# Kernel optimization log

Measured on AMD Instinct MI355X. Metric: run time of the kernel, lower is better.

The kernel has to match this reference:

```python
import jax, jax.numpy as jnp
import numpy as np

OUT = 7            # output_size
SR = 2             # sampling_ratio
SCALES = (0.25, 0.125, 0.0625, 0.03125)   # FPN strides 4,8,16,32
K_MIN, K_MAX = 2, 5
CANON_SCALE = 224.0
CANON_LVL = 4.0
EPS = 1e-6


def setup_inputs() -> dict:
    key = jax.random.key(0)
    ks = jax.random.split(key, 7)
    feat0 = jax.random.normal(ks[0], (2, 256, 200, 200), dtype=jnp.float32)
    feat1 = jax.random.normal(ks[1], (2, 256, 100, 100), dtype=jnp.float32)
    feat2 = jax.random.normal(ks[2], (2, 256, 50, 50), dtype=jnp.float32)
    feat3 = jax.random.normal(ks[3], (2, 256, 25, 25), dtype=jnp.float32)
    # boxes in 800x800 image coords: x1,y1 in [0,600), w,h in [2,200)
    xy = jax.random.uniform(ks[4], (2, 512, 2), dtype=jnp.float32) * 600.0
    wh = jax.random.uniform(ks[5], (2, 512, 2), dtype=jnp.float32) * 198.0 + 2.0
    boxes = jnp.concatenate([xy, xy + wh], axis=-1)  # [B,K,4] x1,y1,x2,y2
    return {"feat0": feat0, "feat1": feat1, "feat2": feat2, "feat3": feat3, "boxes": boxes}


def _bilinear(feat, bidx, ys, xs):
    # feat [B,C,H,W], bidx [N] int, ys [N,OY], xs [N,OX] -> [N,C,OY,OX]
    H, W = feat.shape[2], feat.shape[3]
    vy = (ys >= -1.0) & (ys <= float(H))
    vx = (xs >= -1.0) & (xs <= float(W))
    y = jnp.clip(ys, 0.0, H - 1.0)
    x = jnp.clip(xs, 0.0, W - 1.0)
    y0 = jnp.floor(y).astype(jnp.int32)
    x0 = jnp.floor(x).astype(jnp.int32)
    y1 = jnp.minimum(y0 + 1, H - 1)
    x1 = jnp.minimum(x0 + 1, W - 1)
    ly = y - y0
    lx = x - x0

    def g(yi, xi):
        # advanced indexing -> [N,OY,OX,C]
        return feat[bidx[:, None, None], :, yi[:, :, None], xi[:, None, :]]

    wy0 = (1.0 - ly)[:, :, None, None]
    wy1 = ly[:, :, None, None]
    wx0 = (1.0 - lx)[:, None, :, None]
    wx1 = lx[:, None, :, None]
    v = (wy0 * (wx0 * g(y0, x0) + wx1 * g(y0, x1))
         + wy1 * (wx0 * g(y1, x0) + wx1 * g(y1, x1)))
    v = v * (vy[:, :, None] & vx[:, None, :])[..., None].astype(v.dtype)
    return jnp.transpose(v, (0, 3, 1, 2))  # [N,C,OY,OX]


def _roi_align(feat, bidx, boxes, scale):
    # torchvision roi_align, aligned=False
    x1 = boxes[:, 0] * scale
    y1 = boxes[:, 1] * scale
    x2 = boxes[:, 2] * scale
    y2 = boxes[:, 3] * scale
    rw = jnp.maximum(x2 - x1, 1.0)
    rh = jnp.maximum(y2 - y1, 1.0)
    bw = rw / OUT
    bh = rh / OUT
    # flattened sample offsets: (j + 0.5)/SR in bin units, j in [0, OUT*SR)
    off = (jnp.arange(OUT * SR, dtype=jnp.float32) + 0.5) / SR
    ys = y1[:, None] + off[None, :] * bh[:, None]   # [N, OUT*SR]
    xs = x1[:, None] + off[None, :] * bw[:, None]   # [N, OUT*SR]
    v = _bilinear(feat, bidx, ys, xs)               # [N,C,OUT*SR,OUT*SR]
    N, C = v.shape[0], v.shape[1]
    v = v.reshape(N, C, OUT, SR, OUT, SR)
    return v.mean(axis=(3, 5))                      # [N,C,OUT,OUT]


def reference(feat0, feat1, feat2, feat3, boxes):
    feats = [feat0, feat1, feat2, feat3]
    B, K = boxes.shape[0], boxes.shape[1]
    boxes_f = boxes.reshape(-1, 4)                   # [N,4]
    bidx = jnp.repeat(jnp.arange(B, dtype=jnp.int32), K)
    # FPN level assignment (torchvision LevelMapper)
    area = (boxes_f[:, 2] - boxes_f[:, 0]) * (boxes_f[:, 3] - boxes_f[:, 1])
    lvl = jnp.floor(CANON_LVL + jnp.log2(jnp.sqrt(area) / CANON_SCALE + EPS))
    lvl = jnp.clip(lvl, K_MIN, K_MAX)
    idx = (lvl - K_MIN).astype(jnp.int32)            # [N] in {0..3}
    # compute ROI align at every level, select per box (jit-friendly)
    out = _roi_align(feats[0], bidx, boxes_f, SCALES[0])
    for l in range(1, 4):
        vl = _roi_align(feats[l], bidx, boxes_f, SCALES[l])
        out = jnp.where((idx == l)[:, None, None, None], vl, out)
    return out  # [B*K, C, 7, 7]
```

## Files before the change

kernel.cpp:

```cpp
#include <hip/hip_runtime.h>
#include <math.h>


constexpr int CH = 256;
constexpr int POUT = 7;
constexpr int NSAMP = 14;
constexpr int NBIN = POUT * POUT;
constexpr int PER_ROI = CH * NBIN;
constexpr int NWAVE = 2;
constexpr int CPW = 8;
constexpr int CPB = NWAVE * CPW;
constexpr int NCG = CH / CPB;

struct F2 { float x, y; };
__device__ inline F2 ld2(const float* p) { F2 v; __builtin_memcpy(&v, p, 8); return v; }
struct F4 { float x, y, z, w; };
__device__ inline F4 ld4(const float* p) { F4 v; __builtin_memcpy(&v, p, 16); return v; }

__global__ __launch_bounds__(128)
void roi_align_bin_kernel(const float* __restrict__ f0,
                          const float* __restrict__ f1,
                          const float* __restrict__ f2,
                          const float* __restrict__ f3,
                          const float* __restrict__ boxes,
                          float* __restrict__ out,
                          int K)
{
    __shared__ int   s_rowoff[2 * NSAMP];
    __shared__ float s_wy0[NSAMP], s_wy1[NSAMP];
    __shared__ int   s_xlc[NSAMP];
    __shared__ float s_ex0[NSAMP], s_ex1[NSAMP];

    const int tid  = threadIdx.x;
    const int wave = tid >> 6;
    const int lane = tid & 63;
    const int roi  = blockIdx.x >> 4;
    const int cg   = blockIdx.x & (NCG - 1);
    const int b    = roi / K;

    const float bx1 = boxes[roi * 4 + 0], by1 = boxes[roi * 4 + 1];
    const float bx2 = boxes[roi * 4 + 2], by2 = boxes[roi * 4 + 3];

    const float area = (bx2 - bx1) * (by2 - by1);
    float lvlf = floorf(4.0f + log2f(sqrtf(area) / 224.0f + 1e-6f));
    lvlf = fminf(fmaxf(lvlf, 2.0f), 5.0f);
    const int lvl = (int)lvlf - 2;

    const float* feat; int H, W; float scale;
    if (lvl == 0)      { feat = f0; H = 200; W = 200; scale = 0.25f;    }
    else if (lvl == 1) { feat = f1; H = 100; W = 100; scale = 0.125f;   }
    else if (lvl == 2) { feat = f2; H = 50;  W = 50;  scale = 0.0625f;  }
    else               { feat = f3; H = 25;  W = 25;  scale = 0.03125f; }

    const float x1 = bx1 * scale, y1 = by1 * scale;
    const float rw = fmaxf(bx2 * scale - x1, 1.0f);
    const float rh = fmaxf(by2 * scale - y1, 1.0f);
    const float bw = rw * (1.0f / POUT);
    const float bh = rh * (1.0f / POUT);

    if (tid < 2 * NSAMP) {
        const bool isY = tid < NSAMP;
        const int i = isY ? tid : tid - NSAMP;
        const float dim   = isY ? (float)H : (float)W;
        const float start = isY ? y1 : x1;
        const float bsz   = isY ? bh : bw;
        const float p = start + ((float)i + 0.5f) * 0.5f * bsz;
        const float valid = (p >= -1.0f && p <= dim) ? 1.0f : 0.0f;
        const float pc = fminf(fmaxf(p, 0.0f), dim - 1.0f);
        const int q0 = (int)floorf(pc);
        const float l = pc - (float)q0;
        const float w0 = (1.0f - l) * valid;
        const float w1 = l * valid;
        if (isY) {
            const int q1 = min(q0 + 1, (int)dim - 1);
            s_rowoff[2 * i]     = q0 * W;
            s_rowoff[2 * i + 1] = q1 * W;
            s_wy0[i] = w0;
            s_wy1[i] = w1;
        } else {
            const bool edge = (q0 > W - 2);
            s_xlc[i] = edge ? (W - 2) : q0;
            s_ex0[i] = edge ? 0.0f : w0;
            s_ex1[i] = edge ? (w1 + w0) : w1;
        }
    }
    __syncthreads();

    bool narrow = true;
    #pragma unroll
    for (int j = 0; j < POUT; ++j)
        narrow = narrow && (s_xlc[2 * j + 1] - s_xlc[2 * j] <= 2);

    const int  lp = (lane < NBIN) ? lane : (NBIN - 1);
    const bool act = (lane < NBIN);
    const int  by = lp / POUT, bx = lp - POUT * by;

    const int ro0 = s_rowoff[4 * by + 0];
    const int ro1 = s_rowoff[4 * by + 1];
    const int ro2 = s_rowoff[4 * by + 2];
    const int ro3 = s_rowoff[4 * by + 3];
    const float wy0 = s_wy0[2 * by],     wy1 = s_wy1[2 * by];
    const float wy2 = s_wy0[2 * by + 1], wy3 = s_wy1[2 * by + 1];

    const int lc0 = s_xlc[2 * bx], lc1 = s_xlc[2 * bx + 1];
    const float e00 = s_ex0[2 * bx],     e01 = s_ex1[2 * bx];
    const float e10 = s_ex0[2 * bx + 1], e11 = s_ex1[2 * bx + 1];

    const int HW = H * W;
    const int cbase = cg * CPB + wave * CPW;
    const float* chan0 = feat + ((size_t)b * CH + cbase) * (size_t)HW;
    const size_t obase = (size_t)roi * PER_ROI + (size_t)cbase * NBIN + lp;

    if (narrow) {
        const int base = min(lc0, W - 4);
        const int i0 = lc0 - base;
        const int i1 = lc1 - base;
        const float w40 = (i0 == 0 ? e00 : 0.0f) + (i1 == 0 ? e10 : 0.0f);
        const float w41 = (i0 == 1 ? e00 : 0.0f) + (i0 == 0 ? e01 : 0.0f)
                        + (i1 == 1 ? e10 : 0.0f) + (i1 == 0 ? e11 : 0.0f);
        const float w42 = (i0 == 2 ? e00 : 0.0f) + (i0 == 1 ? e01 : 0.0f)
                        + (i1 == 2 ? e10 : 0.0f) + (i1 == 1 ? e11 : 0.0f);
        const float w43 = (i0 == 2 ? e01 : 0.0f) + (i1 == 2 ? e11 : 0.0f);

        F4 v0 = ld4(chan0 + ro0 + base);
        F4 v1 = ld4(chan0 + ro1 + base);
        F4 v2 = ld4(chan0 + ro2 + base);
        F4 v3 = ld4(chan0 + ro3 + base);

        #pragma unroll
        for (int c = 0; c < CPW; ++c) {
            F4 n0, n1, n2, n3;
            if (c + 1 < CPW) {
                const float* ch = chan0 + (size_t)(c + 1) * HW;
                n0 = ld4(ch + ro0 + base);
                n1 = ld4(ch + ro1 + base);
                n2 = ld4(ch + ro2 + base);
                n3 = ld4(ch + ro3 + base);
            }
            const float rv0 = v0.x * w40 + v0.y * w41 + v0.z * w42 + v0.w * w43;
            const float rv1 = v1.x * w40 + v1.y * w41 + v1.z * w42 + v1.w * w43;
            const float rv2 = v2.x * w40 + v2.y * w41 + v2.z * w42 + v2.w * w43;
            const float rv3 = v3.x * w40 + v3.y * w41 + v3.z * w42 + v3.w * w43;
            const float acc = wy0 * rv0 + wy1 * rv1 + wy2 * rv2 + wy3 * rv3;
            if (act) out[obase + (size_t)c * NBIN] = acc * 0.25f;
            v0 = n0; v1 = n1; v2 = n2; v3 = n3;
        }
    } else {
        F2 a0 = ld2(chan0 + ro0 + lc0), d0 = ld2(chan0 + ro0 + lc1);
        F2 a1 = ld2(chan0 + ro1 + lc0), d1 = ld2(chan0 + ro1 + lc1);
        F2 a2 = ld2(chan0 + ro2 + lc0), d2 = ld2(chan0 + ro2 + lc1);
        F2 a3 = ld2(chan0 + ro3 + lc0), d3 = ld2(chan0 + ro3 + lc1);

        #pragma unroll
        for (int c = 0; c < CPW; ++c) {
            F2 na0, na1, na2, na3, nd0, nd1, nd2, nd3;
            if (c + 1 < CPW) {
                const float* ch = chan0 + (size_t)(c + 1) * HW;
                na0 = ld2(ch + ro0 + lc0); nd0 = ld2(ch + ro0 + lc1);
                na1 = ld2(ch + ro1 + lc0); nd1 = ld2(ch + ro1 + lc1);
                na2 = ld2(ch + ro2 + lc0); nd2 = ld2(ch + ro2 + lc1);
                na3 = ld2(ch + ro3 + lc0); nd3 = ld2(ch + ro3 + lc1);
            }
            const float rv0 = e00 * a0.x + e01 * a0.y + e10 * d0.x + e11 * d0.y;
            const float rv1 = e00 * a1.x + e01 * a1.y + e10 * d1.x + e11 * d1.y;
            const float rv2 = e00 * a2.x + e01 * a2.y + e10 * d2.x + e11 * d2.y;
            const float rv3 = e00 * a3.x + e01 * a3.y + e10 * d3.x + e11 * d3.y;
            const float acc = wy0 * rv0 + wy1 * rv1 + wy2 * rv2 + wy3 * rv3;
            if (act) out[obase + (size_t)c * NBIN] = acc * 0.25f;
            a0 = na0; a1 = na1; a2 = na2; a3 = na3;
            d0 = nd0; d1 = nd1; d2 = nd2; d3 = nd3;
        }
    }
}

extern "C" void kernel_launch(void* const* d_in, const int* in_sizes, int n_in,
                              void* d_out, int out_size, void* d_ws, size_t ws_size,
                              hipStream_t stream) {
    const float* f0    = (const float*)d_in[0];
    const float* f1    = (const float*)d_in[1];
    const float* f2    = (const float*)d_in[2];
    const float* f3    = (const float*)d_in[3];
    const float* boxes = (const float*)d_in[4];
    float* out = (float*)d_out;

    const int B    = in_sizes[0] / (256 * 200 * 200);
    const int nroi = in_sizes[4] / 4;
    const int K    = nroi / B;

    roi_align_bin_kernel<<<nroi * NCG, 128, 0, stream>>>(f0, f1, f2, f3, boxes, out, K);
}
```

Baseline: 64.06 us.

## Stage per-wave outputs in LDS for float4 stores and use 4-wave blocks

Each wave now keeps its 8 channel results in registers, writes them to a per-wave LDS tile, then issues contiguous float4 stores for its 392-float output span. Previously each wave made 8 scalar stores with 49 active lanes. Blocks grow from 2 to 4 waves, halving the block count per ROI. Each wave now computes the shared sample table itself and waits only on its own LDS counter, which drops the block-wide barrier. Every wave writes identical values to the same shared table, so correctness relies on that redundant, unsynchronised write being benign.

```diff
diff --git a/kernel.cpp b/kernel.cpp
--- a/kernel.cpp
+++ b/kernel.cpp
@@ -7,34 +7,36 @@
 constexpr int NSAMP = 14;
 constexpr int NBIN = POUT * POUT;
 constexpr int PER_ROI = CH * NBIN;
-constexpr int NWAVE = 2;
+constexpr int NWAVE = 4;
 constexpr int CPW = 8;
 constexpr int CPB = NWAVE * CPW;
 constexpr int NCG = CH / CPB;
+constexpr int WOUT = CPW * NBIN;
 
 struct F2 { float x, y; };
 __device__ inline F2 ld2(const float* p) { F2 v; __builtin_memcpy(&v, p, 8); return v; }
 struct F4 { float x, y, z, w; };
 __device__ inline F4 ld4(const float* p) { F4 v; __builtin_memcpy(&v, p, 16); return v; }
 
-__global__ __launch_bounds__(128)
-void roi_align_bin_kernel(const float* __restrict__ f0,
-                          const float* __restrict__ f1,
-                          const float* __restrict__ f2,
-                          const float* __restrict__ f3,
-                          const float* __restrict__ boxes,
-                          float* __restrict__ out,
-                          int K)
+__global__ __launch_bounds__(256)
+void roi_align_bin2_kernel(const float* __restrict__ f0,
+                           const float* __restrict__ f1,
+                           const float* __restrict__ f2,
+                           const float* __restrict__ f3,
+                           const float* __restrict__ boxes,
+                           float* __restrict__ out,
+                           int K)
 {
     __shared__ int   s_rowoff[2 * NSAMP];
     __shared__ float s_wy0[NSAMP], s_wy1[NSAMP];
     __shared__ int   s_xlc[NSAMP];
     __shared__ float s_ex0[NSAMP], s_ex1[NSAMP];
+    __shared__ alignas(16) float s_t[NWAVE][WOUT];
 
     const int tid  = threadIdx.x;
     const int wave = tid >> 6;
     const int lane = tid & 63;
-    const int roi  = blockIdx.x >> 4;
+    const int roi  = blockIdx.x >> 3;
     const int cg   = blockIdx.x & (NCG - 1);
     const int b    = roi / K;
 
@@ -58,9 +60,9 @@
     const float bw = rw * (1.0f / POUT);
     const float bh = rh * (1.0f / POUT);
 
-    if (tid < 2 * NSAMP) {
-        const bool isY = tid < NSAMP;
-        const int i = isY ? tid : tid - NSAMP;
+    if (lane < 2 * NSAMP) {
+        const bool isY = lane < NSAMP;
+        const int i = isY ? lane : lane - NSAMP;
         const float dim   = isY ? (float)H : (float)W;
         const float start = isY ? y1 : x1;
         const float bsz   = isY ? bh : bw;
@@ -84,7 +86,8 @@
             s_ex1[i] = edge ? (w1 + w0) : w1;
         }
     }
-    __syncthreads();
+    asm volatile("s_waitcnt lgkmcnt(0)" ::: "memory");
+    __builtin_amdgcn_sched_barrier(0);
 
     bool narrow = true;
     #pragma unroll
@@ -92,7 +95,6 @@
         narrow = narrow && (s_xlc[2 * j + 1] - s_xlc[2 * j] <= 2);
 
     const int  lp = (lane < NBIN) ? lane : (NBIN - 1);
-    const bool act = (lane < NBIN);
     const int  by = lp / POUT, bx = lp - POUT * by;
 
     const int ro0 = s_rowoff[4 * by + 0];
@@ -109,7 +111,8 @@
     const int HW = H * W;
     const int cbase = cg * CPB + wave * CPW;
     const float* chan0 = feat + ((size_t)b * CH + cbase) * (size_t)HW;
-    const size_t obase = (size_t)roi * PER_ROI + (size_t)cbase * NBIN + lp;
+
+    float a[CPW];
 
     if (narrow) {
         const int base = min(lc0, W - 4);
@@ -141,8 +144,7 @@
             const float rv1 = v1.x * w40 + v1.y * w41 + v1.z * w42 + v1.w * w43;
             const float rv2 = v2.x * w40 + v2.y * w41 + v2.z * w42 + v2.w * w43;
             const float rv3 = v3.x * w40 + v3.y * w41 + v3.z * w42 + v3.w * w43;
-            const float acc = wy0 * rv0 + wy1 * rv1 + wy2 * rv2 + wy3 * rv3;
-            if (act) out[obase + (size_t)c * NBIN] = acc * 0.25f;
+            a[c] = (wy0 * rv0 + wy1 * rv1 + wy2 * rv2 + wy3 * rv3) * 0.25f;
             v0 = n0; v1 = n1; v2 = n2; v3 = n3;
         }
     } else {
@@ -165,11 +167,30 @@
             const float rv1 = e00 * a1.x + e01 * a1.y + e10 * d1.x + e11 * d1.y;
             const float rv2 = e00 * a2.x + e01 * a2.y + e10 * d2.x + e11 * d2.y;
             const float rv3 = e00 * a3.x + e01 * a3.y + e10 * d3.x + e11 * d3.y;
-            const float acc = wy0 * rv0 + wy1 * rv1 + wy2 * rv2 + wy3 * rv3;
-            if (act) out[obase + (size_t)c * NBIN] = acc * 0.25f;
+            a[c] = (wy0 * rv0 + wy1 * rv1 + wy2 * rv2 + wy3 * rv3) * 0.25f;
             a0 = na0; a1 = na1; a2 = na2; a3 = na3;
             d0 = nd0; d1 = nd1; d2 = nd2; d3 = nd3;
         }
+    }
+
+    float* wt = s_t[wave];
+    if (lane < NBIN) {
+        #pragma unroll
+        for (int c = 0; c < CPW; ++c)
+            wt[c * NBIN + lane] = a[c];
+    }
+    asm volatile("s_waitcnt lgkmcnt(0)" ::: "memory");
+    __builtin_amdgcn_sched_barrier(0);
+
+    float* wout = out + (size_t)roi * PER_ROI + (size_t)cbase * NBIN;
+    {
+        const float4 v = *(const float4*)(wt + 4 * lane);
+        *(float4*)(wout + 4 * lane) = v;
+    }
+    if (lane < WOUT / 4 - 64) {
+        const int s = 64 + lane;
+        const float4 v = *(const float4*)(wt + 4 * s);
+        *(float4*)(wout + 4 * s) = v;
     }
 }
 
@@ -187,5 +208,5 @@
     const int nroi = in_sizes[4] / 4;
     const int K    = nroi / B;
 
-    roi_align_bin_kernel<<<nroi * NCG, 128, 0, stream>>>(f0, f1, f2, f3, boxes, out, K);
+    roi_align_bin2_kernel<<<nroi * NCG, 256, 0, stream>>>(f0, f1, f2, f3, boxes, out, K);
 }
```

After: 68.85 us. 1.07x slower.
